# Kernel tuning notes

Hardware: AMD Instinct MI355X
Metric: run time of the kernel (lower is better)

Reference implementation:

```python
import jax, jax.numpy as jnp
import numpy as np

B, L, D = 32, 512, 1024

def setup_inputs() -> dict:
    key = jax.random.key(0)
    ks = jax.random.split(key, 9)
    s = 0.02
    return {
        "query": jax.random.normal(ks[0], (B, L, D), jnp.float32),
        "context": jax.random.normal(ks[1], (B, L, D), jnp.float32),
        "W_in": jax.random.normal(ks[2], (D, D), jnp.float32) * s,
        "b_in": jax.random.normal(ks[3], (D,), jnp.float32) * s,
        "W_in2": jax.random.normal(ks[4], (D, D), jnp.float32) * s,
        "b_in2": jax.random.normal(ks[5], (D,), jnp.float32) * s,
        "W_out": jax.random.normal(ks[6], (L, D), jnp.float32) * s,  # windows_lens == L
        "W_fc": jax.random.normal(ks[7], (D, 2 * D), jnp.float32) * s,
        "b_fc": jax.random.normal(ks[8], (D,), jnp.float32) * s,
    }

def reference(query, context, W_in, b_in, W_in2, b_in2, W_out, W_fc, b_fc):
    # additive (Bahdanau) score: tanh(Wq q + Wc c) @ W_out^T -> [B, L, L]
    q = jnp.einsum('bld,ed->ble', query, W_in) + b_in
    c = jnp.einsum('bld,ed->ble', context, W_in2) + b_in2
    alpha = jnp.einsum('bld,wd->blw', jnp.tanh(q + c), W_out)  # [B, L, L]
    alpha = jax.nn.softmax(alpha, axis=-1)
    mix = jnp.einsum('blw,bwd->bld', alpha, context)           # bmm
    cat = jnp.concatenate([mix, context], axis=-1)             # [B, L, 2D]
    out = jnp.einsum('blf,df->bld', cat, W_fc) + b_fc
    return out, alpha
```

## Files before the change

kernel.cpp:

```cpp
#include <hip/hip_runtime.h>
#include <hip/hip_bf16.h>
#include <cstdint>

typedef unsigned short u16;
typedef unsigned int u32;
typedef __bf16 bf16x8 __attribute__((ext_vector_type(8)));
typedef float f32x4 __attribute__((ext_vector_type(4)));
typedef u16 u16x8 __attribute__((ext_vector_type(8)));

#define DEVINL __device__ __forceinline__

typedef __attribute__((address_space(1))) const u32 gbl_u32;
typedef __attribute__((address_space(3))) u32 lds_u32;

DEVINL void llds16(const void* g, void* l) {
  __builtin_amdgcn_global_load_lds((gbl_u32*)g, (lds_u32*)l, 16, 0, 0);
}

DEVINL u16 f2bf(float f) {
  union { float f; u32 i; } x; x.f = f;
  u32 r = x.i + 0x7FFFu + ((x.i >> 16) & 1u);
  return (u16)(r >> 16);
}

DEVINL float fast_tanh(float x) {
  x = fminf(10.f, fmaxf(-10.f, x));
  float e = __expf(2.f * x);
  return (e - 1.f) / (e + 1.f);
}

DEVINL bf16x8 cvt8(const float4& a, const float4& b) {
  bf16x8 r;
  r[0] = (__bf16)a.x; r[1] = (__bf16)a.y; r[2] = (__bf16)a.z; r[3] = (__bf16)a.w;
  r[4] = (__bf16)b.x; r[5] = (__bf16)b.y; r[6] = (__bf16)b.z; r[7] = (__bf16)b.w;
  return r;
}

__global__ __launch_bounds__(256) void cvtk(const float* __restrict__ src,
                                            u16* __restrict__ dst, int n8) {
  int i = blockIdx.x * 256 + threadIdx.x;
  if (i >= n8) return;
  const float* s = src + (size_t)i * 8;
  *(bf16x8*)(dst + (size_t)i * 8) = cvt8(*(const float4*)s, *(const float4*)(s + 4));
}

__global__ __launch_bounds__(256) void tile_b(const float* __restrict__ src,
                                              int srcld, int koff,
                                              u16* __restrict__ dst, int nchunks) {
  int id = blockIdx.x * 256 + threadIdx.x;
  if (id >= nchunks) return;
  int n = id >> 7, k8 = id & 127;
  int kb = k8 >> 2, h = k8 & 3;
  int u = h * 128 + ((n & 127) ^ (h << 1));
  const float* s = src + (size_t)n * srcld + koff + k8 * 8;
  size_t dc = ((size_t)((n >> 7) * 32 + kb) * 512 + u) * 8;
  *(bf16x8*)(dst + dc) = cvt8(*(const float4*)s, *(const float4*)(s + 4));
}

__global__ __launch_bounds__(256) void tile_b64(const float* __restrict__ src,
                                                int srcld, int koff,
                                                u16* __restrict__ dst, int nchunks) {
  int id = blockIdx.x * 256 + threadIdx.x;
  if (id >= nchunks) return;
  int n = id >> 7, k8 = id & 127;
  int kb = k8 >> 3, h = k8 & 7;
  int u = h * 256 + ((n & 255) ^ (h << 1));
  const float* s = src + (size_t)n * srcld + koff + k8 * 8;
  size_t dc = ((size_t)((n >> 8) * 16 + kb) * 2048 + u) * 8;
  *(bf16x8*)(dst + dc) = cvt8(*(const float4*)s, *(const float4*)(s + 4));
}

template <int NSEG, bool OUT_BF16, bool TANH>
__global__ __launch_bounds__(512) void gemm_nt10(
    const u16* __restrict__ A0, const u16* __restrict__ A1,
    const u16* __restrict__ Bt0, const u16* __restrict__ Bt1,
    const float* __restrict__ bias0, const float* __restrict__ bias1,
    void* __restrict__ Cout, int ldc) {
  __shared__ u16 As[3][16384];
  __shared__ u16 Bs[2][16384];
  const int tid = threadIdx.x, lane = tid & 63, w = tid >> 6;
  const int wr = w >> 2, wc = w & 3;

  const int NX = gridDim.x;
  const int total = NX * gridDim.y;
  const int flat = blockIdx.y * NX + blockIdx.x;
  const int wid = (flat & 7) * (total >> 3) + (flat >> 3);
  const int nb = wid % NX;
  const int n0 = nb * 256, m0 = (wid / NX) * 256;

  f32x4 acc[8][4];
#pragma unroll
  for (int i = 0; i < 8; ++i)
#pragma unroll
    for (int j = 0; j < 4; ++j) acc[i][j] = (f32x4)0.f;

  u32 asrc[4], bofs[4];
#pragma unroll
  for (int r = 0; r < 4; ++r) {
    int u = r * 512 + w * 64 + lane;
    int row = u >> 3, oct = (u & 7) ^ (row & 7);
    asrc[r] = (u32)(m0 + row) * 1024u + (u32)(oct * 8);
    bofs[r] = (u32)u * 8u;
  }

  const int NT = NSEG * 16;

  auto stageA = [&](int t) {
    const int seg = (NSEG == 2 && t >= 16) ? 1 : 0;
    const int kb = t - (seg << 4);
    const u16* Ap = seg ? A1 : A0;
    const u32 k0 = (u32)(kb << 6);
    u16* dst = As[t % 3];
#pragma unroll
    for (int q = 0; q < 4; ++q)
      llds16(Ap + (size_t)(asrc[q] + k0), dst + (q * 512 + w * 64) * 8);
  };
  auto stageA2 = [&](int t, int rp) {
    const int seg = (NSEG == 2 && t >= 16) ? 1 : 0;
    const int kb = t - (seg << 4);
    const u16* Ap = seg ? A1 : A0;
    const u32 k0 = (u32)(kb << 6);
    u16* dst = As[t % 3];
#pragma unroll
    for (int r = 0; r < 2; ++r) {
      const int q = rp * 2 + r;
      llds16(Ap + (size_t)(asrc[q] + k0), dst + (q * 512 + w * 64) * 8);
    }
  };
  auto stageB = [&](int t) {
    const int seg = (NSEG == 2 && t >= 16) ? 1 : 0;
    const int kb = t - (seg << 4);
    const u16* Bt = (seg ? Bt1 : Bt0) + ((size_t)(nb * 16 + kb) << 14);
    u16* dst = Bs[t & 1];
#pragma unroll
    for (int q = 0; q < 4; ++q)
      llds16(Bt + (size_t)bofs[q], dst + (q * 512 + w * 64) * 8);
  };
  auto stageB2 = [&](int t, int rp) {
    const int seg = (NSEG == 2 && t >= 16) ? 1 : 0;
    const int kb = t - (seg << 4);
    const u16* Bt = (seg ? Bt1 : Bt0) + ((size_t)(nb * 16 + kb) << 14);
    u16* dst = Bs[t & 1];
#pragma unroll
    for (int r = 0; r < 2; ++r) {
      const int q = rp * 2 + r;
      llds16(Bt + (size_t)bofs[q], dst + (q * 512 + w * 64) * 8);
    }
  };

  stageA(0);
  stageB(0);
  if (NT > 1) stageA(1);
  asm volatile("s_waitcnt vmcnt(6)" ::: "memory");
  __builtin_amdgcn_s_barrier();

  const int rl = lane & 15;
  for (int t = 0; t < NT; ++t) {
    const int ab = t % 3, bb = t & 1;
    const bool preB = (t + 1 < NT);
    const bool preA = (t + 2 < NT);
    bf16x8 af[8];

    {
      const int h = lane >> 4;
      const int jA = h ^ (rl & 7);
#pragma unroll
      for (int i = 0; i < 8; ++i)
        af[i] = *(const bf16x8*)&As[ab][((wr * 128 + i * 16 + rl) * 8 + jA) * 8];
      bf16x8 b0 = *(const bf16x8*)&Bs[bb][(h * 256 + ((wc * 64 + 0 + rl) ^ (h << 1))) * 8];
      bf16x8 b1 = *(const bf16x8*)&Bs[bb][(h * 256 + ((wc * 64 + 16 + rl) ^ (h << 1))) * 8];
      if (preB) stageB2(t + 1, 0);
      __builtin_amdgcn_s_barrier();
      asm volatile("s_waitcnt lgkmcnt(0)" ::: "memory");
      __builtin_amdgcn_sched_barrier(0);
      __builtin_amdgcn_s_setprio(1);
#pragma unroll
      for (int i = 0; i < 8; ++i) {
        acc[i][0] = __builtin_amdgcn_mfma_f32_16x16x32_bf16(af[i], b0, acc[i][0], 0, 0, 0);
        acc[i][1] = __builtin_amdgcn_mfma_f32_16x16x32_bf16(af[i], b1, acc[i][1], 0, 0, 0);
      }
      __builtin_amdgcn_s_setprio(0);
    }
    {
      const int h = lane >> 4;
      bf16x8 b2 = *(const bf16x8*)&Bs[bb][(h * 256 + ((wc * 64 + 32 + rl) ^ (h << 1))) * 8];
      bf16x8 b3 = *(const bf16x8*)&Bs[bb][(h * 256 + ((wc * 64 + 48 + rl) ^ (h << 1))) * 8];
      if (preB) stageB2(t + 1, 1);
      if (preB) asm volatile("s_waitcnt vmcnt(8)" ::: "memory");
      else      asm volatile("s_waitcnt vmcnt(0)" ::: "memory");
      __builtin_amdgcn_s_barrier();
      asm volatile("s_waitcnt lgkmcnt(0)" ::: "memory");
      __builtin_amdgcn_sched_barrier(0);
      __builtin_amdgcn_s_setprio(1);
#pragma unroll
      for (int i = 0; i < 8; ++i) {
        acc[i][2] = __builtin_amdgcn_mfma_f32_16x16x32_bf16(af[i], b2, acc[i][2], 0, 0, 0);
        acc[i][3] = __builtin_amdgcn_mfma_f32_16x16x32_bf16(af[i], b3, acc[i][3], 0, 0, 0);
      }
      __builtin_amdgcn_s_setprio(0);
    }
    {
      const int h = 4 + (lane >> 4);
      const int jA = h ^ (rl & 7);
#pragma unroll
      for (int i = 0; i < 8; ++i)
        af[i] = *(const bf16x8*)&As[ab][((wr * 128 + i * 16 + rl) * 8 + jA) * 8];
      bf16x8 b0 = *(const bf16x8*)&Bs[bb][(h * 256 + ((wc * 64 + 0 + rl) ^ (h << 1))) * 8];
      bf16x8 b1 = *(const bf16x8*)&Bs[bb][(h * 256 + ((wc * 64 + 16 + rl) ^ (h << 1))) * 8];
      if (preA) stageA2(t + 2, 0);
      __builtin_amdgcn_s_barrier();
      asm volatile("s_waitcnt lgkmcnt(0)" ::: "memory");
      __builtin_amdgcn_sched_barrier(0);
      __builtin_amdgcn_s_setprio(1);
#pragma unroll
      for (int i = 0; i < 8; ++i) {
        acc[i][0] = __builtin_amdgcn_mfma_f32_16x16x32_bf16(af[i], b0, acc[i][0], 0, 0, 0);
        acc[i][1] = __builtin_amdgcn_mfma_f32_16x16x32_bf16(af[i], b1, acc[i][1], 0, 0, 0);
      }
      __builtin_amdgcn_s_setprio(0);
    }
    {
      const int h = 4 + (lane >> 4);
      bf16x8 b2 = *(const bf16x8*)&Bs[bb][(h * 256 + ((wc * 64 + 32 + rl) ^ (h << 1))) * 8];
      bf16x8 b3 = *(const bf16x8*)&Bs[bb][(h * 256 + ((wc * 64 + 48 + rl) ^ (h << 1))) * 8];
      if (preA) stageA2(t + 2, 1);
      if (t < NT - 2)       asm volatile("s_waitcnt vmcnt(6)" ::: "memory");
      else if (t == NT - 2) asm volatile("s_waitcnt vmcnt(2)" ::: "memory");
      else                  asm volatile("s_waitcnt vmcnt(0)" ::: "memory");
      __builtin_amdgcn_s_barrier();
      asm volatile("s_waitcnt lgkmcnt(0)" ::: "memory");
      __builtin_amdgcn_sched_barrier(0);
      __builtin_amdgcn_s_setprio(1);
#pragma unroll
      for (int i = 0; i < 8; ++i) {
        acc[i][2] = __builtin_amdgcn_mfma_f32_16x16x32_bf16(af[i], b2, acc[i][2], 0, 0, 0);
        acc[i][3] = __builtin_amdgcn_mfma_f32_16x16x32_bf16(af[i], b3, acc[i][3], 0, 0, 0);
      }
      __builtin_amdgcn_s_setprio(0);
    }
  }

  const int rq = lane >> 4;
#pragma unroll
  for (int j = 0; j < 4; ++j) {
    const int gc = n0 + wc * 64 + j * 16 + rl;
    float bia = 0.f;
    if (bias0) bia += bias0[gc];
    if (NSEG == 2 && bias1) bia += bias1[gc];
#pragma unroll
    for (int i = 0; i < 8; ++i) {
#pragma unroll
      for (int r = 0; r < 4; ++r) {
        const int grow = m0 + wr * 128 + i * 16 + rq * 4 + r;
        float v = acc[i][j][r] + bia;
        if (TANH) v = fast_tanh(v);
        if (OUT_BF16)
          ((u16*)Cout)[(size_t)grow * ldc + gc] = f2bf(v);
        else
          ((float*)Cout)[(size_t)grow * ldc + gc] = v;
      }
    }
  }
}

template <int NSEG, bool OUT_BF16, bool TANH>
__global__ __launch_bounds__(256) void gemm_nt4(
    const u16* __restrict__ A0, const u16* __restrict__ A1, int lda,
    const u16* __restrict__ Bt0, const u16* __restrict__ Bt1,
    const float* __restrict__ bias0, const float* __restrict__ bias1,
    void* __restrict__ Cout, int ldc) {
  __shared__ u16 As[2][4096];
  __shared__ u16 Bs[2][4096];
  const int tid = threadIdx.x, lane = tid & 63, w = tid >> 6;
  const int wr = w >> 1, wc = w & 1;
  const int NX = gridDim.x;
  const int total = NX * gridDim.y;
  const int flat = blockIdx.y * NX + blockIdx.x;
  const int wid = (flat & 7) * (total >> 3) + (flat >> 3);
  const int nb = wid % NX;
  const int n0 = nb * 128, m0 = (wid / NX) * 128;
  const int h = lane >> 4, rl = lane & 15;
  const int jA = h ^ (rl & 3);

  f32x4 acc[4][4];
#pragma unroll
  for (int i = 0; i < 4; ++i)
#pragma unroll
    for (int j = 0; j < 4; ++j) acc[i][j] = (f32x4)0.f;

  const int gb0 = w * 64, gb1 = 256 + w * 64;
  u32 asrc[2];
  {
    int u0 = gb0 + lane, u1 = gb1 + lane;
    int r0 = u0 >> 2, o0 = (u0 & 3) ^ (r0 & 3);
    int r1 = u1 >> 2, o1 = (u1 & 3) ^ (r1 & 3);
    asrc[0] = (u32)(m0 + r0) * (u32)lda + (u32)(o0 * 8);
    asrc[1] = (u32)(m0 + r1) * (u32)lda + (u32)(o1 * 8);
  }
  const int NT = NSEG * 32;

  auto stage = [&](int t, int buf) {
    const int seg = (NSEG == 2 && t >= 32) ? 1 : 0;
    const int kb = t - seg * 32, kl = kb << 5;
    {
      const u16* Bt = (seg ? Bt1 : Bt0) + ((size_t)(nb * 32 + kb) * 512) * 8;
      llds16(Bt + (size_t)(gb0 + lane) * 8, &Bs[buf][gb0 * 8]);
      llds16(Bt + (size_t)(gb1 + lane) * 8, &Bs[buf][gb1 * 8]);
    }
    {
      const u16* Ap = seg ? A1 : A0;
      llds16(Ap + (size_t)(asrc[0] + kl), &As[buf][gb0 * 8]);
      llds16(Ap + (size_t)(asrc[1] + kl), &As[buf][gb1 * 8]);
    }
  };
  auto compute = [&](int buf) {
    bf16x8 af[4], bfv[4];
#pragma unroll
    for (int i = 0; i < 4; ++i)
      af[i] = *(const bf16x8*)&As[buf][((wr * 64 + i * 16 + rl) * 4 + jA) * 8];
#pragma unroll
    for (int j = 0; j < 4; ++j)
      bfv[j] = *(const bf16x8*)&Bs[buf][(h * 128 + ((wc * 64 + j * 16 + rl) ^ (h << 1))) * 8];
#pragma unroll
    for (int i = 0; i < 4; ++i)
#pragma unroll
      for (int j = 0; j < 4; ++j)
        acc[i][j] =
            __builtin_amdgcn_mfma_f32_16x16x32_bf16(af[i], bfv[j], acc[i][j], 0, 0, 0);
  };

  stage(0, 0);
  for (int t = 0; t < NT; ++t) {
    const int c = t & 1;
    if (t + 1 < NT) {
      stage(t + 1, c ^ 1);
      asm volatile("s_waitcnt vmcnt(4)" ::: "memory");
    } else {
      asm volatile("s_waitcnt vmcnt(0)" ::: "memory");
    }
    __builtin_amdgcn_s_barrier();
    __builtin_amdgcn_sched_barrier(0);
    compute(c);
    __builtin_amdgcn_s_barrier();
  }

  const int rq = lane >> 4;
#pragma unroll
  for (int j = 0; j < 4; ++j) {
    const int gc = n0 + wc * 64 + j * 16 + rl;
    float bia = 0.f;
    if (bias0) bia += bias0[gc];
    if (NSEG == 2 && bias1) bia += bias1[gc];
#pragma unroll
    for (int i = 0; i < 4; ++i) {
#pragma unroll
      for (int r = 0; r < 4; ++r) {
        const int grow = m0 + wr * 64 + i * 16 + rq * 4 + r;
        float v = acc[i][j][r] + bia;
        if (TANH) v = fast_tanh(v);
        if (OUT_BF16)
          ((u16*)Cout)[(size_t)grow * ldc + gc] = f2bf(v);
        else
          ((float*)Cout)[(size_t)grow * ldc + gc] = v;
      }
    }
  }
}

__global__ __launch_bounds__(256) void gemm_nn3(
    const float* __restrict__ alpha, const u16* __restrict__ ctxb,
    u16* __restrict__ mix) {
  __shared__ u16 As[2][4096];
  __shared__ u16 Bs[2][4096];
  const int tid = threadIdx.x, lane = tid & 63, w = tid >> 6;
  const int wr = w >> 1, wc = w & 1;
  const int b = blockIdx.z;
  const int n0 = blockIdx.x * 128, m0 = blockIdx.y * 128;
  const int h = lane >> 4, rlx = (lane & 15) ^ (h << 1);
  const float* A = alpha + (size_t)b * 262144;
  u16* C = mix + (size_t)b * 524288;

  f32x4 acc[4][4];
#pragma unroll
  for (int i = 0; i < 4; ++i)
#pragma unroll
    for (int j = 0; j < 4; ++j) acc[i][j] = (f32x4)0.f;

  const int row0 = tid >> 2, cb = tid & 3, row1 = 64 + row0;
  const int unit0 = cb * 128 + (row0 ^ (cb << 1));
  const int unit1 = cb * 128 + (row1 ^ (cb << 1));
  const int kl = tid & 31, ng = tid >> 5;
  const int hb = kl >> 3, kp = kl & 7;

  float4 fr[4];
  u16x8 ub[2];

  auto stage = [&](int t) {
    const int k0 = t << 5;
    const float* p0 = A + (size_t)(m0 + row0) * 512 + k0 + cb * 8;
    const float* p1 = A + (size_t)(m0 + row1) * 512 + k0 + cb * 8;
    fr[0] = *(const float4*)p0; fr[1] = *(const float4*)(p0 + 4);
    fr[2] = *(const float4*)p1; fr[3] = *(const float4*)(p1 + 4);
    const u16* Cb = ctxb + (size_t)b * 524288 + (size_t)(k0 + kl) * 1024 +
                    n0 + ng * 16;
    ub[0] = *(const u16x8*)Cb; ub[1] = *(const u16x8*)(Cb + 8);
  };
  auto stage_fin = [&](int buf) {
    *(bf16x8*)&As[buf][unit0 * 8] = cvt8(fr[0], fr[1]);
    *(bf16x8*)&As[buf][unit1 * 8] = cvt8(fr[2], fr[3]);
#pragma unroll
    for (int j = 0; j < 16; ++j) {
      int n = ng * 16 + j;
      Bs[buf][(hb * 128 + (n ^ (hb << 1))) * 8 + kp] =
          (j < 8) ? ub[0][j] : ub[1][j - 8];
    }
  };
  auto compute = [&](int buf) {
    bf16x8 af[4], bfv[4];
#pragma unroll
    for (int i = 0; i < 4; ++i)
      af[i] = *(const bf16x8*)&As[buf][(h * 128 + wr * 64 + i * 16 + rlx) * 8];
#pragma unroll
    for (int j = 0; j < 4; ++j)
      bfv[j] = *(const bf16x8*)&Bs[buf][(h * 128 + wc * 64 + j * 16 + rlx) * 8];
#pragma unroll
    for (int i = 0; i < 4; ++i)
#pragma unroll
      for (int j = 0; j < 4; ++j)
        acc[i][j] =
            __builtin_amdgcn_mfma_f32_16x16x32_bf16(af[i], bfv[j], acc[i][j], 0, 0, 0);
  };

  stage(0);
  stage_fin(0);
  __syncthreads();
  for (int t = 0; t < 16; ++t) {
    const int cb_ = t & 1;
    if (t + 1 < 16) stage(t + 1);
    compute(cb_);
    if (t + 1 < 16) stage_fin(cb_ ^ 1);
    __syncthreads();
  }

  const int rl = lane & 15, rq = lane >> 4;
#pragma unroll
  for (int j = 0; j < 4; ++j) {
    const int gc = n0 + wc * 64 + j * 16 + rl;
#pragma unroll
    for (int i = 0; i < 4; ++i) {
#pragma unroll
      for (int r = 0; r < 4; ++r) {
        const int grow = m0 + wr * 64 + i * 16 + rq * 4 + r;
        C[(size_t)grow * 1024 + gc] = f2bf(acc[i][j][r]);
      }
    }
  }
}

__global__ __launch_bounds__(256) void softmax_rows_f32(float* __restrict__ S) {
  const int row = blockIdx.x * 4 + (threadIdx.x >> 6);
  const int lane = threadIdx.x & 63;
  float* s = S + (size_t)row * 512 + lane * 8;
  float4 v0 = *(const float4*)s;
  float4 v1 = *(const float4*)(s + 4);
  float vs[8] = {v0.x, v0.y, v0.z, v0.w, v1.x, v1.y, v1.z, v1.w};
  float vm = vs[0];
#pragma unroll
  for (int j = 1; j < 8; ++j) vm = fmaxf(vm, vs[j]);
#pragma unroll
  for (int off = 32; off > 0; off >>= 1) vm = fmaxf(vm, __shfl_xor(vm, off, 64));
  float e[8];
  float sum = 0.f;
#pragma unroll
  for (int j = 0; j < 8; ++j) { e[j] = __expf(vs[j] - vm); sum += e[j]; }
#pragma unroll
  for (int off = 32; off > 0; off >>= 1) sum += __shfl_xor(sum, off, 64);
  float inv = 1.f / sum;
  float4 o0 = {e[0] * inv, e[1] * inv, e[2] * inv, e[3] * inv};
  float4 o1 = {e[4] * inv, e[5] * inv, e[6] * inv, e[7] * inv};
  *(float4*)s = o0;
  *(float4*)(s + 4) = o1;
}

extern "C" void kernel_launch(void* const* d_in, const int* in_sizes, int n_in,
                              void* d_out, int out_size, void* d_ws, size_t ws_size,
                              hipStream_t stream) {
  const float* query = (const float*)d_in[0];
  const float* ctx   = (const float*)d_in[1];
  const float* W_in  = (const float*)d_in[2];
  const float* b_in  = (const float*)d_in[3];
  const float* W_in2 = (const float*)d_in[4];
  const float* b_in2 = (const float*)d_in[5];
  const float* W_out = (const float*)d_in[6];
  const float* W_fc  = (const float*)d_in[7];
  const float* b_fc  = (const float*)d_in[8];

  float* out   = (float*)d_out;
  float* alpha = (float*)d_out + 16777216;

  u16* wibf_t  = (u16*)d_ws;
  u16* wi2bf_t = wibf_t + 1048576;
  u16* wobf_t  = wibf_t + 2097152;
  u16* wf0_t   = wibf_t + 2621440;
  u16* wf1_t   = wibf_t + 3670016;
  u16* t_ws    = (u16*)((char*)d_ws + 9437184);
  u16* cbf     = (u16*)((char*)d_ws + 42991616);
  u16* qbf     = (u16*)((char*)d_ws + 76546048);

  dim3 blk(256, 1, 1);
  dim3 blk5(512, 1, 1);

  tile_b64<<<dim3(512), blk, 0, stream>>>(W_in, 1024, 0, wibf_t, 131072);
  tile_b64<<<dim3(512), blk, 0, stream>>>(W_in2, 1024, 0, wi2bf_t, 131072);
  tile_b<<<dim3(256), blk, 0, stream>>>(W_out, 1024, 0, wobf_t, 65536);
  tile_b64<<<dim3(512), blk, 0, stream>>>(W_fc, 2048, 0, wf0_t, 131072);
  tile_b64<<<dim3(512), blk, 0, stream>>>(W_fc, 2048, 1024, wf1_t, 131072);
  cvtk<<<dim3(8192), blk, 0, stream>>>(ctx, cbf, 2097152);
  cvtk<<<dim3(8192), blk, 0, stream>>>(query, qbf, 2097152);

  gemm_nt10<2, true, true><<<dim3(4, 64), blk5, 0, stream>>>(
      qbf, cbf, wibf_t, wi2bf_t, b_in, b_in2, t_ws, 1024);

  gemm_nt4<1, false, false><<<dim3(4, 128), blk, 0, stream>>>(
      t_ws, nullptr, 1024, wobf_t, nullptr, nullptr, nullptr, alpha, 512);

  softmax_rows_f32<<<dim3(4096), blk, 0, stream>>>(alpha);

  gemm_nn3<<<dim3(8, 4, 32), blk, 0, stream>>>(alpha, cbf, t_ws);

  gemm_nt10<2, false, false><<<dim3(4, 64), blk5, 0, stream>>>(
      t_ws, cbf, wf0_t, wf1_t, b_fc, nullptr, out, 1024);
}
```

Before: 284.4 us.

## Fuse score GEMM with row softmax and merge conversion launches

Replaces the separate score GEMM and softmax kernels with one kernel in which each block computes 64 full rows of 512 scores in registers and applies softmax before writing alpha once. This drops one full write-read round trip of the fp32 alpha matrix. It also merges the five weight-tiling launches into one kernel and the two activation conversions into another, cutting launch count. The trade-offs are a 256-block grid with 128 accumulator registers per thread, which lowers occupancy, and a simpler synchronisation scheme in the K loop.

```diff
diff --git a/kernel.cpp b/kernel.cpp
--- a/kernel.cpp
+++ b/kernel.cpp
@@ -36,38 +36,56 @@
   return r;
 }
 
-__global__ __launch_bounds__(256) void cvtk(const float* __restrict__ src,
-                                            u16* __restrict__ dst, int n8) {
-  int i = blockIdx.x * 256 + threadIdx.x;
-  if (i >= n8) return;
-  const float* s = src + (size_t)i * 8;
-  *(bf16x8*)(dst + (size_t)i * 8) = cvt8(*(const float4*)s, *(const float4*)(s + 4));
-}
-
-__global__ __launch_bounds__(256) void tile_b(const float* __restrict__ src,
-                                              int srcld, int koff,
-                                              u16* __restrict__ dst, int nchunks) {
-  int id = blockIdx.x * 256 + threadIdx.x;
-  if (id >= nchunks) return;
-  int n = id >> 7, k8 = id & 127;
-  int kb = k8 >> 2, h = k8 & 3;
-  int u = h * 128 + ((n & 127) ^ (h << 1));
-  const float* s = src + (size_t)n * srcld + koff + k8 * 8;
-  size_t dc = ((size_t)((n >> 7) * 32 + kb) * 512 + u) * 8;
-  *(bf16x8*)(dst + dc) = cvt8(*(const float4*)s, *(const float4*)(s + 4));
-}
-
-__global__ __launch_bounds__(256) void tile_b64(const float* __restrict__ src,
-                                                int srcld, int koff,
-                                                u16* __restrict__ dst, int nchunks) {
-  int id = blockIdx.x * 256 + threadIdx.x;
-  if (id >= nchunks) return;
+DEVINL void tile64_one(const float* src, int srcld, int koff, u16* dst, int id) {
   int n = id >> 7, k8 = id & 127;
   int kb = k8 >> 3, h = k8 & 7;
   int u = h * 256 + ((n & 255) ^ (h << 1));
   const float* s = src + (size_t)n * srcld + koff + k8 * 8;
-  size_t dc = ((size_t)((n >> 8) * 16 + kb) * 2048 + u) * 8;
-  *(bf16x8*)(dst + dc) = cvt8(*(const float4*)s, *(const float4*)(s + 4));
+  *(bf16x8*)(dst + ((size_t)((n >> 8) * 16 + kb) * 2048 + u) * 8) =
+      cvt8(*(const float4*)s, *(const float4*)(s + 4));
+}
+
+__global__ __launch_bounds__(256) void prep_weights(
+    const float* __restrict__ W_in, const float* __restrict__ W_in2,
+    const float* __restrict__ W_out, const float* __restrict__ W_fc,
+    u16* __restrict__ wibf, u16* __restrict__ wi2bf, u16* __restrict__ wobf,
+    u16* __restrict__ wf0, u16* __restrict__ wf1) {
+  int id = blockIdx.x * 256 + threadIdx.x;
+  if (id < 131072) {
+    tile64_one(W_in, 1024, 0, wibf, id);
+  } else if (id < 262144) {
+    tile64_one(W_in2, 1024, 0, wi2bf, id - 131072);
+  } else if (id < 327680) {
+    int lid = id - 262144;
+    int n = lid >> 7, k8 = lid & 127;
+    int kb = k8 >> 2, h = k8 & 3;
+    int u = h * 128 + ((n & 127) ^ (h << 1));
+    const float* s = W_out + (size_t)n * 1024 + k8 * 8;
+    *(bf16x8*)(wobf + ((size_t)((n >> 7) * 32 + kb) * 512 + u) * 8) =
+        cvt8(*(const float4*)s, *(const float4*)(s + 4));
+  } else if (id < 458752) {
+    tile64_one(W_fc, 2048, 0, wf0, id - 327680);
+  } else if (id < 589824) {
+    tile64_one(W_fc, 2048, 1024, wf1, id - 458752);
+  }
+}
+
+__global__ __launch_bounds__(256) void cvt_acts(const float* __restrict__ ctx,
+                                                const float* __restrict__ query,
+                                                u16* __restrict__ cbf,
+                                                u16* __restrict__ qbf) {
+  int i = blockIdx.x * 256 + threadIdx.x;
+  const float* s;
+  u16* d;
+  if (i < 2097152) {
+    s = ctx + (size_t)i * 8;
+    d = cbf + (size_t)i * 8;
+  } else {
+    int j = i - 2097152;
+    s = query + (size_t)j * 8;
+    d = qbf + (size_t)j * 8;
+  }
+  *(bf16x8*)d = cvt8(*(const float4*)s, *(const float4*)(s + 4));
 }
 
 template <int NSEG, bool OUT_BF16, bool TANH>
@@ -263,107 +281,81 @@
   }
 }
 
-template <int NSEG, bool OUT_BF16, bool TANH>
-__global__ __launch_bounds__(256) void gemm_nt4(
-    const u16* __restrict__ A0, const u16* __restrict__ A1, int lda,
-    const u16* __restrict__ Bt0, const u16* __restrict__ Bt1,
-    const float* __restrict__ bias0, const float* __restrict__ bias1,
-    void* __restrict__ Cout, int ldc) {
-  __shared__ u16 As[2][4096];
-  __shared__ u16 Bs[2][4096];
+__global__ __launch_bounds__(256) void score_softmax(
+    const u16* __restrict__ A, const u16* __restrict__ Bt,
+    float* __restrict__ alpha) {
+  __shared__ u16 As[2][2048];
+  __shared__ u16 Bs[2][16384];
   const int tid = threadIdx.x, lane = tid & 63, w = tid >> 6;
-  const int wr = w >> 1, wc = w & 1;
-  const int NX = gridDim.x;
-  const int total = NX * gridDim.y;
-  const int flat = blockIdx.y * NX + blockIdx.x;
-  const int wid = (flat & 7) * (total >> 3) + (flat >> 3);
-  const int nb = wid % NX;
-  const int n0 = nb * 128, m0 = (wid / NX) * 128;
-  const int h = lane >> 4, rl = lane & 15;
-  const int jA = h ^ (rl & 3);
-
-  f32x4 acc[4][4];
-#pragma unroll
-  for (int i = 0; i < 4; ++i)
-#pragma unroll
-    for (int j = 0; j < 4; ++j) acc[i][j] = (f32x4)0.f;
-
-  const int gb0 = w * 64, gb1 = 256 + w * 64;
-  u32 asrc[2];
-  {
-    int u0 = gb0 + lane, u1 = gb1 + lane;
-    int r0 = u0 >> 2, o0 = (u0 & 3) ^ (r0 & 3);
-    int r1 = u1 >> 2, o1 = (u1 & 3) ^ (r1 & 3);
-    asrc[0] = (u32)(m0 + r0) * (u32)lda + (u32)(o0 * 8);
-    asrc[1] = (u32)(m0 + r1) * (u32)lda + (u32)(o1 * 8);
-  }
-  const int NT = NSEG * 32;
-
-  auto stage = [&](int t, int buf) {
-    const int seg = (NSEG == 2 && t >= 32) ? 1 : 0;
-    const int kb = t - seg * 32, kl = kb << 5;
-    {
-      const u16* Bt = (seg ? Bt1 : Bt0) + ((size_t)(nb * 32 + kb) * 512) * 8;
-      llds16(Bt + (size_t)(gb0 + lane) * 8, &Bs[buf][gb0 * 8]);
-      llds16(Bt + (size_t)(gb1 + lane) * 8, &Bs[buf][gb1 * 8]);
-    }
-    {
-      const u16* Ap = seg ? A1 : A0;
-      llds16(Ap + (size_t)(asrc[0] + kl), &As[buf][gb0 * 8]);
-      llds16(Ap + (size_t)(asrc[1] + kl), &As[buf][gb1 * 8]);
+  const int m0 = blockIdx.x * 64;
+  const int rl = lane & 15, rq = lane >> 4;
+
+  f32x4 acc[32];
+#pragma unroll
+  for (int j = 0; j < 32; ++j) acc[j] = (f32x4)0.f;
+
+  const int arow = tid >> 2;
+  const u32 asrc = (u32)(m0 + arow) * 1024u + (u32)(((tid & 3) ^ (arow & 3)) * 8);
+
+  auto stage = [&](int kb, int buf) {
+    llds16(A + (size_t)(asrc + (u32)(kb << 5)), &As[buf][tid * 8]);
+#pragma unroll
+    for (int p = 0; p < 8; ++p) {
+      int u = p * 256 + tid;
+      int s = u >> 9;
+      llds16(Bt + ((size_t)((s * 32 + kb) * 512 + (u & 511))) * 8,
+             &Bs[buf][(p * 256 + w * 64) * 8]);
     }
   };
   auto compute = [&](int buf) {
-    bf16x8 af[4], bfv[4];
-#pragma unroll
-    for (int i = 0; i < 4; ++i)
-      af[i] = *(const bf16x8*)&As[buf][((wr * 64 + i * 16 + rl) * 4 + jA) * 8];
-#pragma unroll
-    for (int j = 0; j < 4; ++j)
-      bfv[j] = *(const bf16x8*)&Bs[buf][(h * 128 + ((wc * 64 + j * 16 + rl) ^ (h << 1))) * 8];
-#pragma unroll
-    for (int i = 0; i < 4; ++i)
-#pragma unroll
-      for (int j = 0; j < 4; ++j)
-        acc[i][j] =
-            __builtin_amdgcn_mfma_f32_16x16x32_bf16(af[i], bfv[j], acc[i][j], 0, 0, 0);
+    const int h = rq;
+    const int row = w * 16 + rl;
+    bf16x8 af = *(const bf16x8*)&As[buf][(row * 4 + (h ^ (row & 3))) * 8];
+#pragma unroll
+    for (int j = 0; j < 32; ++j) {
+      const int nl = 16 * (j & 7) + rl;
+      const int s = j >> 3;
+      bf16x8 bv = *(const bf16x8*)&Bs[buf][(s * 512 + h * 128 + (nl ^ (h << 1))) * 8];
+      acc[j] = __builtin_amdgcn_mfma_f32_16x16x32_bf16(af, bv, acc[j], 0, 0, 0);
+    }
   };
 
   stage(0, 0);
-  for (int t = 0; t < NT; ++t) {
+  __syncthreads();
+  for (int t = 0; t < 32; ++t) {
     const int c = t & 1;
-    if (t + 1 < NT) {
-      stage(t + 1, c ^ 1);
-      asm volatile("s_waitcnt vmcnt(4)" ::: "memory");
-    } else {
-      asm volatile("s_waitcnt vmcnt(0)" ::: "memory");
-    }
-    __builtin_amdgcn_s_barrier();
-    __builtin_amdgcn_sched_barrier(0);
+    if (t + 1 < 32) stage(t + 1, c ^ 1);
     compute(c);
-    __builtin_amdgcn_s_barrier();
-  }
-
-  const int rq = lane >> 4;
-#pragma unroll
-  for (int j = 0; j < 4; ++j) {
-    const int gc = n0 + wc * 64 + j * 16 + rl;
-    float bia = 0.f;
-    if (bias0) bia += bias0[gc];
-    if (NSEG == 2 && bias1) bia += bias1[gc];
-#pragma unroll
-    for (int i = 0; i < 4; ++i) {
-#pragma unroll
-      for (int r = 0; r < 4; ++r) {
-        const int grow = m0 + wr * 64 + i * 16 + rq * 4 + r;
-        float v = acc[i][j][r] + bia;
-        if (TANH) v = fast_tanh(v);
-        if (OUT_BF16)
-          ((u16*)Cout)[(size_t)grow * ldc + gc] = f2bf(v);
-        else
-          ((float*)Cout)[(size_t)grow * ldc + gc] = v;
-      }
-    }
+    __syncthreads();
+  }
+
+  float inv[4];
+#pragma unroll
+  for (int r = 0; r < 4; ++r) {
+    float m = acc[0][r];
+#pragma unroll
+    for (int j = 1; j < 32; ++j) m = fmaxf(m, acc[j][r]);
+#pragma unroll
+    for (int mask = 1; mask < 16; mask <<= 1)
+      m = fmaxf(m, __shfl_xor(m, mask, 64));
+    float s = 0.f;
+#pragma unroll
+    for (int j = 0; j < 32; ++j) {
+      acc[j][r] = __expf(acc[j][r] - m);
+      s += acc[j][r];
+    }
+#pragma unroll
+    for (int mask = 1; mask < 16; mask <<= 1) s += __shfl_xor(s, mask, 64);
+    inv[r] = 1.f / s;
+  }
+
+  const int growb = m0 + w * 16 + rq * 4;
+#pragma unroll
+  for (int j = 0; j < 32; ++j) {
+    const int gc = j * 16 + rl;
+#pragma unroll
+    for (int r = 0; r < 4; ++r)
+      alpha[(size_t)(growb + r) * 512 + gc] = acc[j][r] * inv[r];
   }
 }
 
@@ -457,31 +449,6 @@
   }
 }
 
-__global__ __launch_bounds__(256) void softmax_rows_f32(float* __restrict__ S) {
-  const int row = blockIdx.x * 4 + (threadIdx.x >> 6);
-  const int lane = threadIdx.x & 63;
-  float* s = S + (size_t)row * 512 + lane * 8;
-  float4 v0 = *(const float4*)s;
-  float4 v1 = *(const float4*)(s + 4);
-  float vs[8] = {v0.x, v0.y, v0.z, v0.w, v1.x, v1.y, v1.z, v1.w};
-  float vm = vs[0];
-#pragma unroll
-  for (int j = 1; j < 8; ++j) vm = fmaxf(vm, vs[j]);
-#pragma unroll
-  for (int off = 32; off > 0; off >>= 1) vm = fmaxf(vm, __shfl_xor(vm, off, 64));
-  float e[8];
-  float sum = 0.f;
-#pragma unroll
-  for (int j = 0; j < 8; ++j) { e[j] = __expf(vs[j] - vm); sum += e[j]; }
-#pragma unroll
-  for (int off = 32; off > 0; off >>= 1) sum += __shfl_xor(sum, off, 64);
-  float inv = 1.f / sum;
-  float4 o0 = {e[0] * inv, e[1] * inv, e[2] * inv, e[3] * inv};
-  float4 o1 = {e[4] * inv, e[5] * inv, e[6] * inv, e[7] * inv};
-  *(float4*)s = o0;
-  *(float4*)(s + 4) = o1;
-}
-
 extern "C" void kernel_launch(void* const* d_in, const int* in_sizes, int n_in,
                               void* d_out, int out_size, void* d_ws, size_t ws_size,
                               hipStream_t stream) {
@@ -510,21 +477,15 @@
   dim3 blk(256, 1, 1);
   dim3 blk5(512, 1, 1);
 
-  tile_b64<<<dim3(512), blk, 0, stream>>>(W_in, 1024, 0, wibf_t, 131072);
-  tile_b64<<<dim3(512), blk, 0, stream>>>(W_in2, 1024, 0, wi2bf_t, 131072);
-  tile_b<<<dim3(256), blk, 0, stream>>>(W_out, 1024, 0, wobf_t, 65536);
-  tile_b64<<<dim3(512), blk, 0, stream>>>(W_fc, 2048, 0, wf0_t, 131072);
-  tile_b64<<<dim3(512), blk, 0, stream>>>(W_fc, 2048, 1024, wf1_t, 131072);
-  cvtk<<<dim3(8192), blk, 0, stream>>>(ctx, cbf, 2097152);
-  cvtk<<<dim3(8192), blk, 0, stream>>>(query, qbf, 2097152);
+  prep_weights<<<dim3(2304), blk, 0, stream>>>(W_in, W_in2, W_out, W_fc,
+                                               wibf_t, wi2bf_t, wobf_t, wf0_t,
+                                               wf1_t);
+  cvt_acts<<<dim3(16384), blk, 0, stream>>>(ctx, query, cbf, qbf);
 
   gemm_nt10<2, true, true><<<dim3(4, 64), blk5, 0, stream>>>(
       qbf, cbf, wibf_t, wi2bf_t, b_in, b_in2, t_ws, 1024);
 
-  gemm_nt4<1, false, false><<<dim3(4, 128), blk, 0, stream>>>(
-      t_ws, nullptr, 1024, wobf_t, nullptr, nullptr, nullptr, alpha, 512);
-
-  softmax_rows_f32<<<dim3(4096), blk, 0, stream>>>(alpha);
+  score_softmax<<<dim3(256), blk, 0, stream>>>(t_ws, wobf_t, alpha);
 
   gemm_nn3<<<dim3(8, 4, 32), blk, 0, stream>>>(alpha, cbf, t_ws);
 
```

After: 285.4 us. No clear change (+0.3%).
